# Kernel tuning notes

Hardware: AMD Instinct MI355X
Metric: run time of the kernel (lower is better)

The kernel has to match this reference:

```python
import jax, jax.numpy as jnp
import numpy as np

DIM, HEADS, KV_HEADS = 1024, 16, 4
B, T = 1, 4096
HEAD_DIM = DIM // HEADS           # 64
KV_DIM = DIM // (HEADS // KV_HEADS)  # 256
SCALE = HEAD_DIM ** -0.5


def setup_inputs() -> dict:
    key = jax.random.key(0)
    ks = jax.random.split(key, 9)
    s = lambda fan_in: fan_in ** -0.5
    return {
        "x": jax.random.normal(ks[0], (B, T, DIM), jnp.float32),
        "mask": jnp.tril(jnp.ones((1, 1, T, T), jnp.bool_)),  # causal
        "q_w": jax.random.normal(ks[1], (DIM, DIM), jnp.float32) * s(DIM),
        "q_b": jnp.zeros((DIM,), jnp.float32),
        "k_w": jax.random.normal(ks[2], (KV_DIM, DIM), jnp.float32) * s(DIM),
        "k_b": jnp.zeros((KV_DIM,), jnp.float32),
        "v_w": jax.random.normal(ks[3], (KV_DIM, DIM), jnp.float32) * s(DIM),
        "v_b": jnp.zeros((KV_DIM,), jnp.float32),
        "o_w": jax.random.normal(ks[4], (DIM, DIM), jnp.float32) * s(DIM),
        "o_b": jnp.zeros((DIM,), jnp.float32),
    }


def reference(x, mask, q_w, q_b, k_w, k_b, v_w, v_b, o_w, o_b):
    b, t, d = x.shape
    g = HEADS // KV_HEADS  # query heads per kv head
    # projections (torch Linear: x @ W^T + b)
    q = (x @ q_w.T + q_b).reshape(b, t, HEADS, HEAD_DIM).transpose(0, 2, 1, 3)      # [B,H,T,hd]
    k = (x @ k_w.T + k_b).reshape(b, t, KV_HEADS, HEAD_DIM).transpose(0, 2, 1, 3)   # [B,Hk,T,hd]
    v = (x @ v_w.T + v_b).reshape(b, t, KV_HEADS, HEAD_DIM).transpose(0, 2, 1, 3)   # [B,Hk,T,hd]
    # GQA: group query heads over shared kv heads
    qg = q.reshape(b, KV_HEADS, g, t, HEAD_DIM)                                     # [B,Hk,g,T,hd]
    scores = jnp.einsum('bkgtd,bksd->bkgts', qg, k) * SCALE                         # [B,Hk,g,T,T]
    scores = jnp.where(mask[:, :, None, :, :], scores, -1e9)
    attn = jax.nn.softmax(scores, axis=-1)  # dropout is identity in eval mode
    out = jnp.einsum('bkgts,bksd->bkgtd', attn, v)                                  # [B,Hk,g,T,hd]
    out = out.reshape(b, HEADS, t, HEAD_DIM).transpose(0, 2, 1, 3).reshape(b, t, d)
    out = out @ o_w.T + o_b
    return out, k, v  # (output, new kv cache)
```

## Files before the change

kernel.cpp:

```cpp
#include <hip/hip_runtime.h>
#include <hip/hip_bf16.h>
#include <stdint.h>

typedef __bf16 bf16;
typedef __bf16 bf16x8 __attribute__((ext_vector_type(8)));
typedef __bf16 bf16x4 __attribute__((ext_vector_type(4)));
typedef float  f32x4 __attribute__((ext_vector_type(4)));

#define SEQ   4096
#define DIM_  1024
#define HD_   64
#define NEG_BIG (-30000.0f)

#define QSCALE (0.125f * 1.4426950408889634f)

__device__ __forceinline__ bf16x8 cvt8(const float* p) {
    f32x4 a = *(const f32x4*)p, b = *(const f32x4*)(p + 4);
    bf16x8 r;
    r[0]=(bf16)a[0]; r[1]=(bf16)a[1]; r[2]=(bf16)a[2]; r[3]=(bf16)a[3];
    r[4]=(bf16)b[0]; r[5]=(bf16)b[1]; r[6]=(bf16)b[2]; r[7]=(bf16)b[3];
    return r;
}

__device__ __forceinline__ void gload16(const bf16* g, bf16* l) {
    __builtin_amdgcn_global_load_lds(
        (const __attribute__((address_space(1))) void*)g,
        (__attribute__((address_space(3))) void*)l, 16, 0, 0);
}

__global__ __launch_bounds__(256)
void conv_bf16(const float* __restrict__ x,  const float* __restrict__ qw,
               const float* __restrict__ kw, const float* __restrict__ vw,
               const float* __restrict__ ow,
               bf16* __restrict__ xb,  bf16* __restrict__ qwb,
               bf16* __restrict__ kwb, bf16* __restrict__ vwb,
               bf16* __restrict__ owb)
{
    int b = blockIdx.x;
    const float* s; bf16* d; int base;
    if (b < 2048)      { s = x;  d = xb;  base = b * 2048; }
    else if (b < 2560) { s = qw; d = qwb; base = (b - 2048) * 2048; }
    else if (b < 2688) { s = kw; d = kwb; base = (b - 2560) * 2048; }
    else if (b < 2816) { s = vw; d = vwb; base = (b - 2688) * 2048; }
    else               { s = ow; d = owb; base = (b - 2816) * 2048; }
    int i = base + threadIdx.x * 8;
    *(bf16x8*)(d + i) = cvt8(s + i);
}

template<int MODE, bool BWBF>
__global__ __launch_bounds__(256)
void gemm_bt(const bf16* __restrict__ A,
             const void* __restrict__ B0, const float* __restrict__ b0,
             const void* __restrict__ B1, const float* __restrict__ b1,
             const void* __restrict__ B2, const float* __restrict__ b2,
             float* __restrict__ C0, float* __restrict__ C1, float* __restrict__ C2,
             bf16* __restrict__ Qbf, bf16* __restrict__ Kbf, bf16* __restrict__ VTbf)
{
    const int K = 1024;
    const int tid  = threadIdx.x;
    const int lane = tid & 63, wave = tid >> 6;
    const int qd = lane >> 4, ln = lane & 15;
    const int wm = (wave & 1) * 32, wn = (wave >> 1) * 64;
    const int m0 = blockIdx.x * 64, n0 = blockIdx.y * 128;

    const void* Bp; const float* bias;
    if (MODE == 1) {
        if (n0 < 1024)      { Bp = (const bf16*)B0 + (size_t)n0 * K;        bias = b0 + n0; }
        else if (n0 < 1280) { Bp = (const bf16*)B1 + (size_t)(n0-1024) * K; bias = b1 + (n0-1024); }
        else                { Bp = (const bf16*)B2 + (size_t)(n0-1280) * K; bias = b2 + (n0-1280); }
    } else if (BWBF)        { Bp = (const bf16*)B0 + (size_t)n0 * K;        bias = b0 + n0; }
    else                    { Bp = (const float*)B0 + (size_t)n0 * K;       bias = b0 + n0; }

    __shared__ bf16 As[64*32];
    __shared__ bf16 Bs[128*32];

    const int gr = lane >> 2, gc = (lane & 3) * 8;
    const bf16* Ag  = A + (size_t)(m0 + wave*16 + gr) * K + gc;
    bf16* AsW = As + wave*16*32;
    const bf16* Bg0 = (const bf16*)Bp + (size_t)(wave*32 + gr) * K + gc;
    const bf16* Bg1 = (const bf16*)Bp + (size_t)(wave*32 + 16 + gr) * K + gc;
    bf16* BsW0 = Bs + (wave*32) * 32;
    bf16* BsW1 = Bs + (wave*32 + 16) * 32;

    f32x4 acc[2][4] = {};

    for (int k0 = 0; k0 < K; k0 += 32) {
        if constexpr (MODE == 1 || BWBF) {
            __syncthreads();
            gload16(Ag  + k0, AsW);
            gload16(Bg0 + k0, BsW0);
            gload16(Bg1 + k0, BsW1);
            __syncthreads();
        } else {
            bf16x8 rb[2];
            #pragma unroll
            for (int i = 0; i < 2; ++i) {
                int s = i*256 + tid;
                int row = s >> 2, ch = s & 3;
                rb[i] = cvt8((const float*)Bp + (size_t)row*K + k0 + ch*8);
            }
            __syncthreads();
            gload16(Ag + k0, AsW);
            #pragma unroll
            for (int i = 0; i < 2; ++i) {
                int s = i*256 + tid;
                int row = s >> 2, ch = s & 3;
                *(bf16x8*)(Bs + row*32 + ch*8) = rb[i];
            }
            __syncthreads();
        }

        bf16x8 af[2], bg[4];
        #pragma unroll
        for (int i = 0; i < 2; ++i)
            af[i] = *(const bf16x8*)(As + (wm + i*16 + ln)*32 + qd*8);
        #pragma unroll
        for (int j = 0; j < 4; ++j)
            bg[j] = *(const bf16x8*)(Bs + (wn + j*16 + ln)*32 + qd*8);

        #pragma unroll
        for (int i = 0; i < 2; ++i)
            #pragma unroll
            for (int j = 0; j < 4; ++j)
                acc[i][j] = __builtin_amdgcn_mfma_f32_16x16x32_bf16(af[i], bg[j], acc[i][j], 0, 0, 0);
    }

    #pragma unroll
    for (int i = 0; i < 2; ++i) {
        #pragma unroll
        for (int j = 0; j < 4; ++j) {
            int colg = n0 + wn + j*16 + ln;
            float bv = bias[wn + j*16 + ln];
            #pragma unroll
            for (int r = 0; r < 4; ++r) {
                int rowg = m0 + wm + i*16 + qd*4 + r;
                float v = acc[i][j][r] + bv;
                if (MODE == 0) {
                    C0[(size_t)rowg*1024 + colg] = v;
                } else if (colg < 1024) {
                    Qbf[(size_t)rowg*1024 + colg] = (bf16)(v * QSCALE);
                } else if (colg < 1280) {
                    int c2 = colg - 1024;
                    size_t idx = (size_t)(c2 >> 6)*(SEQ*HD_) + (size_t)rowg*HD_ + (c2 & 63);
                    C1[idx]  = v;
                    Kbf[idx] = (bf16)v;
                } else {
                    int c2 = colg - 1280;
                    C2[(size_t)(c2 >> 6)*(SEQ*HD_) + (size_t)rowg*HD_ + (c2 & 63)] = v;
                    VTbf[(size_t)(c2 >> 6)*(HD_*SEQ) + (size_t)(c2 & 63)*SEQ + rowg] = (bf16)v;
                }
            }
        }
    }
}

__global__ __launch_bounds__(256)
void attn_fwd(const bf16* __restrict__ Q, const bf16* __restrict__ Kc,
              const bf16* __restrict__ VT, bf16* __restrict__ att)
{
    const int bid  = blockIdx.x;
    const int head = bid & 15;
    const int mt   = 63 - (bid >> 4);
    const int qb   = mt * 64;
    const int kvh  = head >> 2;

    const int tid = threadIdx.x, lane = tid & 63, wave = tid >> 6;
    const int qd = lane >> 4, ln = lane & 15;
    const int rw0 = qb + wave * 16;

    __shared__ bf16 Ks[64*72];
    __shared__ bf16 Vt[64*72];
    __shared__ bf16 Ps[4][16*72];
    __shared__ float Lr[4][16];

    const bf16* Kbase = Kc + (size_t)kvh * SEQ * HD_;
    const bf16* Vbase = VT + (size_t)kvh * HD_ * SEQ;

    bf16x8 aq[2];
    #pragma unroll
    for (int ks = 0; ks < 2; ++ks)
        aq[ks] = *(const bf16x8*)(Q + (size_t)(rw0 + ln)*DIM_ + head*HD_ + ks*32 + qd*8);

    f32x4 o[4] = {};
    float l_lane = 0.f;

    const float C16 = 16.0f * 1.4426950408889634f;
    const int nkt = mt + 1;

    for (int kt = 0; kt < nkt; ++kt) {
        const int kb = kt * 64;

        bf16x8 rk[2], rv[2];
        #pragma unroll
        for (int i = 0; i < 2; ++i) {
            int s = i*256 + tid;
            int r8 = s >> 3, ch = s & 7;
            rk[i] = *(const bf16x8*)(Kbase + (size_t)(kb + r8)*HD_ + ch*8);
            rv[i] = *(const bf16x8*)(Vbase + (size_t)r8*SEQ + kb + ch*8);
        }
        __syncthreads();
        #pragma unroll
        for (int i = 0; i < 2; ++i) {
            int s = i*256 + tid;
            int r8 = s >> 3, ch = s & 7;
            *(bf16x8*)(Ks + r8*72 + ch*8) = rk[i];
            *(bf16x8*)(Vt + r8*72 + ch*8) = rv[i];
        }
        __syncthreads();

        f32x4 S[4] = {};
        #pragma unroll
        for (int ks = 0; ks < 2; ++ks) {
            bf16x8 bk[4];
            #pragma unroll
            for (int nf = 0; nf < 4; ++nf)
                bk[nf] = *(const bf16x8*)(Ks + (nf*16 + ln)*72 + ks*32 + qd*8);
            #pragma unroll
            for (int nf = 0; nf < 4; ++nf)
                S[nf] = __builtin_amdgcn_mfma_f32_16x16x32_bf16(bk[nf], aq[ks], S[nf], 0, 0, 0);
        }

        if (kt == nkt - 1) {
            int qrow = rw0 + ln;
            #pragma unroll
            for (int nf = 0; nf < 4; ++nf) {
                #pragma unroll
                for (int r = 0; r < 4; ++r) {
                    int kcol = kb + nf*16 + qd*4 + r;
                    if (kcol > qrow) S[nf][r] = NEG_BIG;
                }
            }
        }

        bf16* Pw = &Ps[wave][0];
        #pragma unroll
        for (int nf = 0; nf < 4; ++nf) {
            bf16x4 pk;
            #pragma unroll
            for (int r = 0; r < 4; ++r) {
                float p = exp2f(S[nf][r] - C16);
                l_lane += p;
                pk[r] = (bf16)p;
            }
            *(bf16x4*)(Pw + ln*72 + nf*16 + qd*4) = pk;
        }
        asm volatile("s_waitcnt lgkmcnt(0)" ::: "memory");

        #pragma unroll
        for (int ks = 0; ks < 2; ++ks) {
            bf16x8 bv[4];
            #pragma unroll
            for (int nf = 0; nf < 4; ++nf)
                bv[nf] = *(const bf16x8*)(Vt + (nf*16 + ln)*72 + ks*32 + qd*8);
            bf16x8 ap = *(const bf16x8*)(&Ps[wave][ln*72 + ks*32 + qd*8]);
            #pragma unroll
            for (int nf = 0; nf < 4; ++nf)
                o[nf] = __builtin_amdgcn_mfma_f32_16x16x32_bf16(ap, bv[nf], o[nf], 0, 0, 0);
        }
    }

    l_lane += __shfl_xor(l_lane, 16);
    l_lane += __shfl_xor(l_lane, 32);
    Lr[wave][ln] = l_lane;
    asm volatile("s_waitcnt lgkmcnt(0)" ::: "memory");
    #pragma unroll
    for (int r = 0; r < 4; ++r) {
        float inv = 1.0f / Lr[wave][qd*4 + r];
        int trow = rw0 + qd*4 + r;
        #pragma unroll
        for (int nf = 0; nf < 4; ++nf)
            att[(size_t)trow*DIM_ + head*HD_ + nf*16 + ln] = (bf16)(o[nf][r] * inv);
    }
}

extern "C" void kernel_launch(void* const* d_in, const int* in_sizes, int n_in,
                              void* d_out, int out_size, void* d_ws, size_t ws_size,
                              hipStream_t stream)
{
    const float* x  = (const float*)d_in[0];
    const float* qw = (const float*)d_in[2];
    const float* qb = (const float*)d_in[3];
    const float* kw = (const float*)d_in[4];
    const float* kb = (const float*)d_in[5];
    const float* vw = (const float*)d_in[6];
    const float* vb = (const float*)d_in[7];
    const float* ow = (const float*)d_in[8];
    const float* ob = (const float*)d_in[9];

    float* out  = (float*)d_out;
    float* kout = out  + (size_t)SEQ * DIM_;
    float* vout = kout + (size_t)4 * SEQ * HD_;

    bf16* q_bf  = (bf16*)d_out;
    bf16* k_bf  = q_bf  + (size_t)SEQ * DIM_;
    bf16* vT_bf = k_bf  + (size_t)4 * SEQ * HD_;
    bf16* qw_bf = vT_bf + (size_t)4 * HD_ * SEQ;
    bf16* kw_bf = qw_bf + (size_t)1024 * 1024;
    bf16* vw_bf = kw_bf + (size_t)256 * 1024;

    bf16* x_bf = (bf16*)d_ws;
    bf16* att  = (bf16*)d_ws;
    bool  owbf_ok = ws_size >= (size_t)(8*1024*1024 + 2*1024*1024);
    bf16* ow_bf = owbf_ok ? (bf16*)((char*)d_ws + (size_t)8*1024*1024) : nullptr;

    int convBlocks = 2816 + (owbf_ok ? 512 : 0);
    conv_bf16<<<convBlocks, 256, 0, stream>>>(x, qw, kw, vw, ow,
                                              x_bf, qw_bf, kw_bf, vw_bf, ow_bf);

    gemm_bt<1, true><<<dim3(64, 12), 256, 0, stream>>>(x_bf, qw_bf, qb, kw_bf, kb, vw_bf, vb,
                                                       nullptr, kout, vout,
                                                       q_bf, k_bf, vT_bf);
    attn_fwd<<<dim3(1024), 256, 0, stream>>>(q_bf, k_bf, vT_bf, att);
    if (owbf_ok)
        gemm_bt<0, true><<<dim3(64, 8), 256, 0, stream>>>(att, ow_bf, ob, nullptr, nullptr,
                                                          nullptr, nullptr, out, nullptr, nullptr,
                                                          nullptr, nullptr, nullptr);
    else
        gemm_bt<0, false><<<dim3(64, 8), 256, 0, stream>>>(att, ow, ob, nullptr, nullptr,
                                                           nullptr, nullptr, out, nullptr, nullptr,
                                                           nullptr, nullptr, nullptr);
}
```

Measured before the change: 247.5 us.

## Double-buffer LDS tiles in bf16 GEMM with async global-to-LDS prefetch

For the bf16-weight GEMM paths, LDS tiles are now double-buffered. The loads for tile t+2 are issued while tile t is being computed, and the code waits on them with explicit vmcnt counters instead of a full __syncthreads around each load. The aim is to overlap global memory latency with MFMA work. The cost is twice the LDS use per block, and correctness now depends on the hand-counted vmcnt values matching the outstanding loads per stage.

```diff
diff --git a/kernel.cpp b/kernel.cpp
--- a/kernel.cpp
+++ b/kernel.cpp
@@ -56,7 +56,7 @@
              float* __restrict__ C0, float* __restrict__ C1, float* __restrict__ C2,
              bf16* __restrict__ Qbf, bf16* __restrict__ Kbf, bf16* __restrict__ VTbf)
 {
-    const int K = 1024;
+    const int K = 1024, NT = 32;
     const int tid  = threadIdx.x;
     const int lane = tid & 63, wave = tid >> 6;
     const int qd = lane >> 4, ln = lane & 15;
@@ -71,27 +71,54 @@
     } else if (BWBF)        { Bp = (const bf16*)B0 + (size_t)n0 * K;        bias = b0 + n0; }
     else                    { Bp = (const float*)B0 + (size_t)n0 * K;       bias = b0 + n0; }
 
-    __shared__ bf16 As[64*32];
-    __shared__ bf16 Bs[128*32];
+    __shared__ bf16 As[2][64*32];
+    __shared__ bf16 Bs[2][128*32];
 
     const int gr = lane >> 2, gc = (lane & 3) * 8;
     const bf16* Ag  = A + (size_t)(m0 + wave*16 + gr) * K + gc;
-    bf16* AsW = As + wave*16*32;
     const bf16* Bg0 = (const bf16*)Bp + (size_t)(wave*32 + gr) * K + gc;
     const bf16* Bg1 = (const bf16*)Bp + (size_t)(wave*32 + 16 + gr) * K + gc;
-    bf16* BsW0 = Bs + (wave*32) * 32;
-    bf16* BsW1 = Bs + (wave*32 + 16) * 32;
+    const int aW = (wave*16) * 32;
+    const int bW0 = (wave*32) * 32, bW1 = (wave*32 + 16) * 32;
 
     f32x4 acc[2][4] = {};
 
-    for (int k0 = 0; k0 < K; k0 += 32) {
-        if constexpr (MODE == 1 || BWBF) {
-            __syncthreads();
-            gload16(Ag  + k0, AsW);
-            gload16(Bg0 + k0, BsW0);
-            gload16(Bg1 + k0, BsW1);
-            __syncthreads();
-        } else {
+    if constexpr (MODE == 1 || BWBF) {
+        auto stage = [&](int buf, int t) {
+            int k0 = t * 32;
+            gload16(Ag  + k0, &As[buf][aW]);
+            gload16(Bg0 + k0, &Bs[buf][bW0]);
+            gload16(Bg1 + k0, &Bs[buf][bW1]);
+        };
+        stage(0, 0);
+        stage(1, 1);
+        for (int t = 0; t < NT; ++t) {
+            const int cur = t & 1;
+            if (t < NT - 1) asm volatile("s_waitcnt vmcnt(3)" ::: "memory");
+            else            asm volatile("s_waitcnt vmcnt(0)" ::: "memory");
+            __builtin_amdgcn_s_barrier();
+
+            bf16x8 af[2], bg[4];
+            #pragma unroll
+            for (int i = 0; i < 2; ++i)
+                af[i] = *(const bf16x8*)(&As[cur][(wm + i*16 + ln)*32 + qd*8]);
+            #pragma unroll
+            for (int j = 0; j < 4; ++j)
+                bg[j] = *(const bf16x8*)(&Bs[cur][(wn + j*16 + ln)*32 + qd*8]);
+            #pragma unroll
+            for (int i = 0; i < 2; ++i)
+                #pragma unroll
+                for (int j = 0; j < 4; ++j)
+                    acc[i][j] = __builtin_amdgcn_mfma_f32_16x16x32_bf16(af[i], bg[j], acc[i][j], 0, 0, 0);
+
+            if (t + 2 < NT) {
+                __builtin_amdgcn_s_barrier();
+                stage(cur, t + 2);
+            }
+        }
+    } else {
+        for (int t = 0; t < NT; ++t) {
+            int k0 = t * 32;
             bf16x8 rb[2];
             #pragma unroll
             for (int i = 0; i < 2; ++i) {
@@ -100,29 +127,27 @@
                 rb[i] = cvt8((const float*)Bp + (size_t)row*K + k0 + ch*8);
             }
             __syncthreads();
-            gload16(Ag + k0, AsW);
+            gload16(Ag + k0, &As[0][aW]);
             #pragma unroll
             for (int i = 0; i < 2; ++i) {
                 int s = i*256 + tid;
                 int row = s >> 2, ch = s & 3;
-                *(bf16x8*)(Bs + row*32 + ch*8) = rb[i];
+                *(bf16x8*)(&Bs[0][row*32 + ch*8]) = rb[i];
             }
             __syncthreads();
-        }
-
-        bf16x8 af[2], bg[4];
-        #pragma unroll
-        for (int i = 0; i < 2; ++i)
-            af[i] = *(const bf16x8*)(As + (wm + i*16 + ln)*32 + qd*8);
-        #pragma unroll
-        for (int j = 0; j < 4; ++j)
-            bg[j] = *(const bf16x8*)(Bs + (wn + j*16 + ln)*32 + qd*8);
-
-        #pragma unroll
-        for (int i = 0; i < 2; ++i)
+            bf16x8 af[2], bg[4];
+            #pragma unroll
+            for (int i = 0; i < 2; ++i)
+                af[i] = *(const bf16x8*)(&As[0][(wm + i*16 + ln)*32 + qd*8]);
             #pragma unroll
             for (int j = 0; j < 4; ++j)
-                acc[i][j] = __builtin_amdgcn_mfma_f32_16x16x32_bf16(af[i], bg[j], acc[i][j], 0, 0, 0);
+                bg[j] = *(const bf16x8*)(&Bs[0][(wn + j*16 + ln)*32 + qd*8]);
+            #pragma unroll
+            for (int i = 0; i < 2; ++i)
+                #pragma unroll
+                for (int j = 0; j < 4; ++j)
+                    acc[i][j] = __builtin_amdgcn_mfma_f32_16x16x32_bf16(af[i], bg[j], acc[i][j], 0, 0, 0);
+        }
     }
 
     #pragma unroll
```

Result: faster. 242.6 us (-2.0%).
